# Optimization experiments

Measured on AMD Instinct MI355X. Metric: run time of the kernel, lower is better.

## Reference

```python
import jax, jax.numpy as jnp
import numpy as np

B, S, H = 32, 2048, 1024

def setup_inputs() -> dict:
    key = jax.random.key(0)
    ks = jax.random.split(key, 8)
    s = 1.0 / np.sqrt(H)
    return {
        "query": jax.random.normal(ks[0], (B, 1, H), jnp.float32),
        "keys": jax.random.normal(ks[1], (B, S, H), jnp.float32),
        "Wa_w": jax.random.normal(ks[2], (H, H), jnp.float32) * s,
        "Wa_b": jax.random.normal(ks[3], (H,), jnp.float32) * s,
        "Ua_w": jax.random.normal(ks[4], (H, H), jnp.float32) * s,
        "Ua_b": jax.random.normal(ks[5], (H,), jnp.float32) * s,
        "Va_w": jax.random.normal(ks[6], (1, H), jnp.float32) * s,
        "Va_b": jax.random.normal(ks[7], (1,), jnp.float32) * s,
    }

def reference(query, keys, Wa_w, Wa_b, Ua_w, Ua_b, Va_w, Va_b):
    # Wa(query): (B,1,H); Ua(keys): (B,S,H); broadcast add -> (B,S,H)
    q = jnp.einsum('bqh,oh->bqo', query, Wa_w) + Wa_b
    k = jnp.einsum('bsh,oh->bso', keys, Ua_w) + Ua_b
    h = jnp.tanh(q + k)                              # (B,S,H)
    scores = jnp.einsum('bsh,oh->bso', h, Va_w) + Va_b  # (B,S,1)
    scores = scores[:, :, 0][:, None, :]             # (B,1,S)
    weights = jax.nn.softmax(scores, axis=-1)        # (B,1,S)
    context = jnp.einsum('bqs,bsh->bqh', weights, keys)  # (B,1,H)
    return context, weights
```

## Files before the change

kernel.cpp:

```cpp
#include <hip/hip_runtime.h>
#include <hip/hip_bf16.h>

#define HDIM 1024
#define SEQ  2048
#define BATCH 32
#define M_TOTAL (BATCH * SEQ)
#define BM 256
#define BN 128
#define BK 32
#define NSLICE 16

typedef __bf16 bf16x8 __attribute__((ext_vector_type(8)));
typedef float  f32x4  __attribute__((ext_vector_type(4)));
typedef unsigned short u16;
#define AS1 __attribute__((address_space(1)))
#define AS3 __attribute__((address_space(3)))

__device__ __forceinline__ u16 f2bf(float f) {
    unsigned int u = __float_as_uint(f);
    u += 0x7FFFu + ((u >> 16) & 1u);
    return (u16)(u >> 16);
}

__global__ __launch_bounds__(256) void cvt_kernel(const float* __restrict__ in,
                                                  u16* __restrict__ out) {
    size_t i = ((size_t)blockIdx.x * 256 + threadIdx.x) * 8;
    float4 f0 = *(const float4*)(in + i);
    float4 f1 = *(const float4*)(in + i + 4);
    uint4 v;
    v.x = (unsigned)f2bf(f0.x) | ((unsigned)f2bf(f0.y) << 16);
    v.y = (unsigned)f2bf(f0.z) | ((unsigned)f2bf(f0.w) << 16);
    v.z = (unsigned)f2bf(f1.x) | ((unsigned)f2bf(f1.y) << 16);
    v.w = (unsigned)f2bf(f1.z) | ((unsigned)f2bf(f1.w) << 16);
    *(uint4*)(out + i) = v;
}

__global__ __launch_bounds__(256) void qb_kernel(const float* __restrict__ query,
                                                 const float* __restrict__ Wa_w,
                                                 const float* __restrict__ Wa_b,
                                                 const float* __restrict__ Ua_b,
                                                 float* __restrict__ qb) {
    __shared__ float qs[HDIM];
    const int b = blockIdx.x;
    const int tid = threadIdx.x;
    ((float4*)qs)[tid] = ((const float4*)(query + b * HDIM))[tid];
    __syncthreads();
    const int lane = tid & 63;
    const int w = tid >> 6;
    const int obase = blockIdx.y * 64 + w * 16;
    for (int i = 0; i < 16; i++) {
        int o = obase + i;
        const float4* wrow = (const float4*)(Wa_w + (size_t)o * HDIM);
        float s = 0.f;
        #pragma unroll
        for (int j = 0; j < 4; j++) {
            float4 wv = wrow[j * 64 + lane];
            float4 qv = ((const float4*)qs)[j * 64 + lane];
            s += wv.x * qv.x + wv.y * qv.y + wv.z * qv.z + wv.w * qv.w;
        }
        #pragma unroll
        for (int m = 1; m < 64; m <<= 1) s += __shfl_xor(s, m);
        if (lane == 0) qb[b * HDIM + o] = s + Wa_b[o] + Ua_b[o];
    }
}

__global__ __launch_bounds__(256, 2) void gemm_score_kernel(const u16* __restrict__ keysb,
                                                            const u16* __restrict__ uab,
                                                            const float* __restrict__ qb,
                                                            const float* __restrict__ vaw,
                                                            float* __restrict__ sp) {
    __shared__ __align__(16) u16 As[BM * BK];
    __shared__ __align__(16) u16 Bs[BN * BK];
    const int tid  = threadIdx.x;
    const int lane = tid & 63;
    const int w    = tid >> 6;
    const int m0 = blockIdx.x * BM;
    const int n0 = blockIdx.y * BN;
    const int wave_m = (w & 1) * 128;
    const int wave_n = (w >> 1) * 64;

    f32x4 acc[8][4] = {};

    const int srow = lane >> 2;
    const int scol = (lane & 3) * 8;
    const u16* gA = keysb + (size_t)(m0 + w * 64 + srow) * HDIM + scol;
    const u16* gB = uab   + (size_t)(n0 + w * 32 + srow) * HDIM + scol;
    u16* lA = As + (w * 64) * BK;
    u16* lB = Bs + (w * 32) * BK;

    const int fr = lane & 15;
    const int fq = lane >> 4;

    for (int k0 = 0; k0 < HDIM; k0 += BK) {
        __syncthreads();
        #pragma unroll
        for (int i = 0; i < 4; i++)
            __builtin_amdgcn_global_load_lds((AS1 void*)(gA + k0 + i * 16 * HDIM),
                                             (AS3 void*)(lA + i * 16 * BK), 16, 0, 0);
        #pragma unroll
        for (int i = 0; i < 2; i++)
            __builtin_amdgcn_global_load_lds((AS1 void*)(gB + k0 + i * 16 * HDIM),
                                             (AS3 void*)(lB + i * 16 * BK), 16, 0, 0);
        __syncthreads();

        bf16x8 a[8], b[4];
        #pragma unroll
        for (int i = 0; i < 8; i++)
            a[i] = *(const bf16x8*)(As + (wave_m + i * 16 + fr) * BK + fq * 8);
        #pragma unroll
        for (int i = 0; i < 4; i++)
            b[i] = *(const bf16x8*)(Bs + (wave_n + i * 16 + fr) * BK + fq * 8);
        #pragma unroll
        for (int mi = 0; mi < 8; mi++)
            #pragma unroll
            for (int ni = 0; ni < 4; ni++)
                acc[mi][ni] = __builtin_amdgcn_mfma_f32_16x16x32_bf16(a[mi], b[ni], acc[mi][ni], 0, 0, 0);
    }

    const int bidx = m0 >> 11;
    float qv[4], vv[4];
    #pragma unroll
    for (int ni = 0; ni < 4; ni++) {
        int n_g = n0 + wave_n + ni * 16 + fr;
        qv[ni] = qb[bidx * HDIM + n_g];
        vv[ni] = vaw[n_g];
    }
    const int slice = blockIdx.y * 2 + (w >> 1);
    float* sl = sp + ((size_t)slice * BATCH + bidx) * SEQ;
    #pragma unroll
    for (int mi = 0; mi < 8; mi++) {
        #pragma unroll
        for (int r = 0; r < 4; r++) {
            float p = 0.f;
            #pragma unroll
            for (int ni = 0; ni < 4; ni++) {
                float x = acc[mi][ni][r] + qv[ni];
                float e = __expf(2.f * x);
                p += (1.f - 2.f / (e + 1.f)) * vv[ni];
            }
            p += __shfl_xor(p, 1);
            p += __shfl_xor(p, 2);
            p += __shfl_xor(p, 4);
            p += __shfl_xor(p, 8);
            if (fr == 0) {
                int s_g = (m0 + wave_m + mi * 16 + fq * 4 + r) & (SEQ - 1);
                sl[s_g] = p;
            }
        }
    }
}

__global__ __launch_bounds__(256) void softmax_kernel(const float* __restrict__ sp,
                                                      float* __restrict__ weights,
                                                      float* __restrict__ ctx) {
    __shared__ float red[4];
    const int b = blockIdx.x;
    const int tid = threadIdx.x;
    float4 z = {0.f, 0.f, 0.f, 0.f};
    ((float4*)(ctx + b * HDIM))[tid] = z;
    float v[8];
    float mx = -1e30f;
    #pragma unroll
    for (int i = 0; i < 8; i++) {
        int s = tid + i * 256;
        float a = 0.f;
        #pragma unroll
        for (int j = 0; j < NSLICE; j++) a += sp[((size_t)j * BATCH + b) * SEQ + s];
        v[i] = a;
        mx = fmaxf(mx, a);
    }
    #pragma unroll
    for (int m = 1; m < 64; m <<= 1) mx = fmaxf(mx, __shfl_xor(mx, m));
    if ((tid & 63) == 0) red[tid >> 6] = mx;
    __syncthreads();
    mx = fmaxf(fmaxf(red[0], red[1]), fmaxf(red[2], red[3]));
    float sum = 0.f;
    #pragma unroll
    for (int i = 0; i < 8; i++) { v[i] = __expf(v[i] - mx); sum += v[i]; }
    #pragma unroll
    for (int m = 1; m < 64; m <<= 1) sum += __shfl_xor(sum, m);
    __syncthreads();
    if ((tid & 63) == 0) red[tid >> 6] = sum;
    __syncthreads();
    sum = red[0] + red[1] + red[2] + red[3];
    float inv = 1.f / sum;
    #pragma unroll
    for (int i = 0; i < 8; i++) weights[b * SEQ + tid + i * 256] = v[i] * inv;
}

__global__ __launch_bounds__(256) void context_kernel(const float* __restrict__ keys,
                                                      const float* __restrict__ weights,
                                                      float* __restrict__ ctx) {
    __shared__ float wsm[64];
    const int b = blockIdx.x;
    const int s0 = blockIdx.y * 64;
    const int tid = threadIdx.x;
    if (tid < 64) wsm[tid] = weights[b * SEQ + s0 + tid];
    __syncthreads();
    float ax = 0.f, ay = 0.f, az = 0.f, aw = 0.f;
    const float4* kp = (const float4*)(keys + (size_t)b * SEQ * HDIM + (size_t)s0 * HDIM) + tid;
    #pragma unroll 8
    for (int s = 0; s < 64; s++) {
        float4 kv = kp[s * 256];
        float wv = wsm[s];
        ax += wv * kv.x; ay += wv * kv.y; az += wv * kv.z; aw += wv * kv.w;
    }
    float* o = ctx + b * HDIM + tid * 4;
    atomicAdd(o + 0, ax);
    atomicAdd(o + 1, ay);
    atomicAdd(o + 2, az);
    atomicAdd(o + 3, aw);
}

extern "C" void kernel_launch(void* const* d_in, const int* in_sizes, int n_in,
                              void* d_out, int out_size, void* d_ws, size_t ws_size,
                              hipStream_t stream) {
    const float* query = (const float*)d_in[0];
    const float* keys  = (const float*)d_in[1];
    const float* Wa_w  = (const float*)d_in[2];
    const float* Wa_b  = (const float*)d_in[3];
    const float* Ua_w  = (const float*)d_in[4];
    const float* Ua_b  = (const float*)d_in[5];
    const float* Va_w  = (const float*)d_in[6];
    float* out = (float*)d_out;

    char* ws = (char*)d_ws;
    u16*  keysb = (u16*)ws;
    u16*  uab   = (u16*)(ws + 134217728);
    float* qb   = (float*)(ws + 134217728 + 2097152);
    float* sp   = (float*)(ws + 134217728 + 2097152 + 131072);

    cvt_kernel<<<(BATCH * SEQ * HDIM) / 2048, 256, 0, stream>>>(keys, keysb);
    cvt_kernel<<<(HDIM * HDIM) / 2048, 256, 0, stream>>>(Ua_w, uab);
    qb_kernel<<<dim3(BATCH, HDIM / 64), 256, 0, stream>>>(query, Wa_w, Wa_b, Ua_b, qb);
    gemm_score_kernel<<<dim3(M_TOTAL / BM, HDIM / BN), 256, 0, stream>>>(keysb, uab, qb, Va_w, sp);
    softmax_kernel<<<BATCH, 256, 0, stream>>>(sp, out + BATCH * HDIM, out);
    context_kernel<<<dim3(BATCH, SEQ / 64), 256, 0, stream>>>(keys, out + BATCH * HDIM, out);
}
```

Baseline: 671.9 us.

## Fuse fp32-to-bf16 key conversion into GEMM loads, shrink tile, swizzle LDS

Drops the separate pass that converted the full keys tensor to bf16. The GEMM now loads fp32 keys straight into LDS and converts them to bf16 in registers before the MFMA, which removes the 256MB read plus 128MB write of the conversion pass. To fit the doubled fp32 A tile, BM drops from 256 to 128 and the occupancy hint rises to 3. The grid is reordered so N-blocks sharing an M tile run together, and XOR swizzles are added to LDS accesses to cut bank conflicts. In exchange, the GEMM reads fp32 keys once per N block (8 times in total), which doubles its A-side global traffic, and it adds conversion work inside the inner loop.

```diff
diff --git a/kernel.cpp b/kernel.cpp
--- a/kernel.cpp
+++ b/kernel.cpp
@@ -5,7 +5,7 @@
 #define SEQ  2048
 #define BATCH 32
 #define M_TOTAL (BATCH * SEQ)
-#define BM 256
+#define BM 128
 #define BN 128
 #define BK 32
 #define NSLICE 16
@@ -20,6 +20,15 @@
     unsigned int u = __float_as_uint(f);
     u += 0x7FFFu + ((u >> 16) & 1u);
     return (u16)(u >> 16);
+}
+
+__device__ __forceinline__ bf16x8 cvt8(float4 f0, float4 f1) {
+    union { bf16x8 v; __hip_bfloat162 h[4]; } u;
+    u.h[0] = __float22bfloat162_rn({f0.x, f0.y});
+    u.h[1] = __float22bfloat162_rn({f0.z, f0.w});
+    u.h[2] = __float22bfloat162_rn({f1.x, f1.y});
+    u.h[3] = __float22bfloat162_rn({f1.z, f1.w});
+    return u.v;
 }
 
 __global__ __launch_bounds__(256) void cvt_kernel(const float* __restrict__ in,
@@ -64,54 +73,61 @@
     }
 }
 
-__global__ __launch_bounds__(256, 2) void gemm_score_kernel(const u16* __restrict__ keysb,
+__global__ __launch_bounds__(256, 3) void gemm_score_kernel(const float* __restrict__ keys,
                                                             const u16* __restrict__ uab,
                                                             const float* __restrict__ qb,
                                                             const float* __restrict__ vaw,
                                                             float* __restrict__ sp) {
-    __shared__ __align__(16) u16 As[BM * BK];
-    __shared__ __align__(16) u16 Bs[BN * BK];
+    __shared__ __align__(16) float As[BM * BK];
+    __shared__ __align__(16) u16   Bs[BN * BK];
     const int tid  = threadIdx.x;
     const int lane = tid & 63;
     const int w    = tid >> 6;
-    const int m0 = blockIdx.x * BM;
-    const int n0 = blockIdx.y * BN;
-    const int wave_m = (w & 1) * 128;
+    const int n0 = blockIdx.x * BN;
+    const int m0 = blockIdx.y * BM;
+    const int wave_m = (w & 1) * 64;
     const int wave_n = (w >> 1) * 64;
 
-    f32x4 acc[8][4] = {};
-
-    const int srow = lane >> 2;
-    const int scol = (lane & 3) * 8;
-    const u16* gA = keysb + (size_t)(m0 + w * 64 + srow) * HDIM + scol;
-    const u16* gB = uab   + (size_t)(n0 + w * 32 + srow) * HDIM + scol;
-    u16* lA = As + (w * 64) * BK;
+    f32x4 acc[4][4] = {};
+
+    const int arow = lane >> 3;
+    const int achk = (lane & 7) ^ (arow & 7);
+    const float* gA = keys + (size_t)(m0 + w * 32 + arow) * HDIM + achk * 4;
+    float* lA = As + (w * 32) * BK;
+    const int brow = lane >> 2;
+    const int bchk = (lane & 3) ^ ((lane >> 3) & 3);
+    const u16* gB = uab + (size_t)(n0 + w * 32 + brow) * HDIM + bchk * 8;
     u16* lB = Bs + (w * 32) * BK;
 
     const int fr = lane & 15;
     const int fq = lane >> 4;
+    const int aswz0 = ((2 * fq + 0) ^ (fr & 7)) * 4;
+    const int aswz1 = ((2 * fq + 1) ^ (fr & 7)) * 4;
+    const int bswz  = (fq ^ ((fr >> 1) & 3)) * 8;
 
     for (int k0 = 0; k0 < HDIM; k0 += BK) {
         __syncthreads();
         #pragma unroll
         for (int i = 0; i < 4; i++)
-            __builtin_amdgcn_global_load_lds((AS1 void*)(gA + k0 + i * 16 * HDIM),
-                                             (AS3 void*)(lA + i * 16 * BK), 16, 0, 0);
+            __builtin_amdgcn_global_load_lds((AS1 void*)(gA + k0 + i * 8 * HDIM),
+                                             (AS3 void*)(lA + i * 8 * BK), 16, 0, 0);
         #pragma unroll
         for (int i = 0; i < 2; i++)
             __builtin_amdgcn_global_load_lds((AS1 void*)(gB + k0 + i * 16 * HDIM),
                                              (AS3 void*)(lB + i * 16 * BK), 16, 0, 0);
         __syncthreads();
 
-        bf16x8 a[8], b[4];
-        #pragma unroll
-        for (int i = 0; i < 8; i++)
-            a[i] = *(const bf16x8*)(As + (wave_m + i * 16 + fr) * BK + fq * 8);
-        #pragma unroll
-        for (int i = 0; i < 4; i++)
-            b[i] = *(const bf16x8*)(Bs + (wave_n + i * 16 + fr) * BK + fq * 8);
-        #pragma unroll
-        for (int mi = 0; mi < 8; mi++)
+        bf16x8 a[4], b[4];
+        #pragma unroll
+        for (int i = 0; i < 4; i++) {
+            const float* ar = As + (wave_m + i * 16 + fr) * BK;
+            float4 f0 = *(const float4*)(ar + aswz0);
+            float4 f1 = *(const float4*)(ar + aswz1);
+            a[i] = cvt8(f0, f1);
+            b[i] = *(const bf16x8*)(Bs + (wave_n + i * 16 + fr) * BK + bswz);
+        }
+        #pragma unroll
+        for (int mi = 0; mi < 4; mi++)
             #pragma unroll
             for (int ni = 0; ni < 4; ni++)
                 acc[mi][ni] = __builtin_amdgcn_mfma_f32_16x16x32_bf16(a[mi], b[ni], acc[mi][ni], 0, 0, 0);
@@ -125,10 +141,10 @@
         qv[ni] = qb[bidx * HDIM + n_g];
         vv[ni] = vaw[n_g];
     }
-    const int slice = blockIdx.y * 2 + (w >> 1);
+    const int slice = blockIdx.x * 2 + (w >> 1);
     float* sl = sp + ((size_t)slice * BATCH + bidx) * SEQ;
     #pragma unroll
-    for (int mi = 0; mi < 8; mi++) {
+    for (int mi = 0; mi < 4; mi++) {
         #pragma unroll
         for (int r = 0; r < 4; r++) {
             float p = 0.f;
@@ -225,15 +241,13 @@
     float* out = (float*)d_out;
 
     char* ws = (char*)d_ws;
-    u16*  keysb = (u16*)ws;
-    u16*  uab   = (u16*)(ws + 134217728);
-    float* qb   = (float*)(ws + 134217728 + 2097152);
-    float* sp   = (float*)(ws + 134217728 + 2097152 + 131072);
-
-    cvt_kernel<<<(BATCH * SEQ * HDIM) / 2048, 256, 0, stream>>>(keys, keysb);
+    u16*  uab = (u16*)ws;
+    float* qb = (float*)(ws + 2097152);
+    float* sp = (float*)(ws + 2097152 + 131072);
+
     cvt_kernel<<<(HDIM * HDIM) / 2048, 256, 0, stream>>>(Ua_w, uab);
     qb_kernel<<<dim3(BATCH, HDIM / 64), 256, 0, stream>>>(query, Wa_w, Wa_b, Ua_b, qb);
-    gemm_score_kernel<<<dim3(M_TOTAL / BM, HDIM / BN), 256, 0, stream>>>(keysb, uab, qb, Va_w, sp);
+    gemm_score_kernel<<<dim3(HDIM / BN, M_TOTAL / BM), 256, 0, stream>>>(keys, uab, qb, Va_w, sp);
     softmax_kernel<<<BATCH, 256, 0, stream>>>(sp, out + BATCH * HDIM, out);
     context_kernel<<<dim3(BATCH, SEQ / 64), 256, 0, stream>>>(keys, out + BATCH * HDIM, out);
 }
```

Measured after the change: 644.0 us. 1.04x faster.

## Swap GEMM tile shape and grid order; read bf16 keys in context kernel

Applied to the files above, without the earlier changes.

The GEMM tile changes from 256x128 to 128x256, and the grid is reordered so N-blocks vary fastest. Consecutive blocks then share the same keys rows in cache, and fewer score slices are written. The context kernel now reads the bf16 copy of keys instead of the fp32 original, halving the bytes of its main memory stream. The cost is reduced precision in the context output and more atomic adds per block.

```diff
diff --git a/kernel.cpp b/kernel.cpp
--- a/kernel.cpp
+++ b/kernel.cpp
@@ -5,10 +5,10 @@
 #define SEQ  2048
 #define BATCH 32
 #define M_TOTAL (BATCH * SEQ)
-#define BM 256
-#define BN 128
+#define BM 128
+#define BN 256
 #define BK 32
-#define NSLICE 16
+#define NSLICE 8
 
 typedef __bf16 bf16x8 __attribute__((ext_vector_type(8)));
 typedef float  f32x4  __attribute__((ext_vector_type(4)));
@@ -74,19 +74,19 @@
     const int tid  = threadIdx.x;
     const int lane = tid & 63;
     const int w    = tid >> 6;
-    const int m0 = blockIdx.x * BM;
-    const int n0 = blockIdx.y * BN;
-    const int wave_m = (w & 1) * 128;
-    const int wave_n = (w >> 1) * 64;
-
-    f32x4 acc[8][4] = {};
+    const int n0 = blockIdx.x * BN;
+    const int m0 = blockIdx.y * BM;
+    const int wave_m = (w & 1) * 64;
+    const int wave_n = (w >> 1) * 128;
+
+    f32x4 acc[4][8] = {};
 
     const int srow = lane >> 2;
     const int scol = (lane & 3) * 8;
-    const u16* gA = keysb + (size_t)(m0 + w * 64 + srow) * HDIM + scol;
-    const u16* gB = uab   + (size_t)(n0 + w * 32 + srow) * HDIM + scol;
-    u16* lA = As + (w * 64) * BK;
-    u16* lB = Bs + (w * 32) * BK;
+    const u16* gA = keysb + (size_t)(m0 + w * 32 + srow) * HDIM + scol;
+    const u16* gB = uab   + (size_t)(n0 + w * 64 + srow) * HDIM + scol;
+    u16* lA = As + (w * 32) * BK;
+    u16* lB = Bs + (w * 64) * BK;
 
     const int fr = lane & 15;
     const int fq = lane >> 4;
@@ -94,46 +94,46 @@
     for (int k0 = 0; k0 < HDIM; k0 += BK) {
         __syncthreads();
         #pragma unroll
-        for (int i = 0; i < 4; i++)
+        for (int i = 0; i < 2; i++)
             __builtin_amdgcn_global_load_lds((AS1 void*)(gA + k0 + i * 16 * HDIM),
                                              (AS3 void*)(lA + i * 16 * BK), 16, 0, 0);
         #pragma unroll
-        for (int i = 0; i < 2; i++)
+        for (int i = 0; i < 4; i++)
             __builtin_amdgcn_global_load_lds((AS1 void*)(gB + k0 + i * 16 * HDIM),
                                              (AS3 void*)(lB + i * 16 * BK), 16, 0, 0);
         __syncthreads();
 
-        bf16x8 a[8], b[4];
+        bf16x8 a[4], b[8];
+        #pragma unroll
+        for (int i = 0; i < 4; i++)
+            a[i] = *(const bf16x8*)(As + (wave_m + i * 16 + fr) * BK + fq * 8);
         #pragma unroll
         for (int i = 0; i < 8; i++)
-            a[i] = *(const bf16x8*)(As + (wave_m + i * 16 + fr) * BK + fq * 8);
-        #pragma unroll
-        for (int i = 0; i < 4; i++)
             b[i] = *(const bf16x8*)(Bs + (wave_n + i * 16 + fr) * BK + fq * 8);
         #pragma unroll
-        for (int mi = 0; mi < 8; mi++)
+        for (int mi = 0; mi < 4; mi++)
             #pragma unroll
-            for (int ni = 0; ni < 4; ni++)
+            for (int ni = 0; ni < 8; ni++)
                 acc[mi][ni] = __builtin_amdgcn_mfma_f32_16x16x32_bf16(a[mi], b[ni], acc[mi][ni], 0, 0, 0);
     }
 
     const int bidx = m0 >> 11;
-    float qv[4], vv[4];
-    #pragma unroll
-    for (int ni = 0; ni < 4; ni++) {
+    float qv[8], vv[8];
+    #pragma unroll
+    for (int ni = 0; ni < 8; ni++) {
         int n_g = n0 + wave_n + ni * 16 + fr;
         qv[ni] = qb[bidx * HDIM + n_g];
         vv[ni] = vaw[n_g];
     }
-    const int slice = blockIdx.y * 2 + (w >> 1);
+    const int slice = blockIdx.x * 2 + (w >> 1);
     float* sl = sp + ((size_t)slice * BATCH + bidx) * SEQ;
     #pragma unroll
-    for (int mi = 0; mi < 8; mi++) {
+    for (int mi = 0; mi < 4; mi++) {
         #pragma unroll
         for (int r = 0; r < 4; r++) {
             float p = 0.f;
             #pragma unroll
-            for (int ni = 0; ni < 4; ni++) {
+            for (int ni = 0; ni < 8; ni++) {
                 float x = acc[mi][ni][r] + qv[ni];
                 float e = __expf(2.f * x);
                 p += (1.f - 2.f / (e + 1.f)) * vv[ni];
@@ -188,7 +188,7 @@
     for (int i = 0; i < 8; i++) weights[b * SEQ + tid + i * 256] = v[i] * inv;
 }
 
-__global__ __launch_bounds__(256) void context_kernel(const float* __restrict__ keys,
+__global__ __launch_bounds__(256) void context_kernel(const u16* __restrict__ keysb,
                                                       const float* __restrict__ weights,
                                                       float* __restrict__ ctx) {
     __shared__ float wsm[64];
@@ -197,19 +197,34 @@
     const int tid = threadIdx.x;
     if (tid < 64) wsm[tid] = weights[b * SEQ + s0 + tid];
     __syncthreads();
-    float ax = 0.f, ay = 0.f, az = 0.f, aw = 0.f;
-    const float4* kp = (const float4*)(keys + (size_t)b * SEQ * HDIM + (size_t)s0 * HDIM) + tid;
+    const int hq = tid & 127;
+    const int sh = (tid >> 7) * 32;
+    float a0 = 0.f, a1 = 0.f, a2 = 0.f, a3 = 0.f;
+    float a4 = 0.f, a5 = 0.f, a6 = 0.f, a7 = 0.f;
+    const uint4* kp = (const uint4*)(keysb + (size_t)b * SEQ * HDIM
+                                     + (size_t)(s0 + sh) * HDIM) + hq;
     #pragma unroll 8
-    for (int s = 0; s < 64; s++) {
-        float4 kv = kp[s * 256];
-        float wv = wsm[s];
-        ax += wv * kv.x; ay += wv * kv.y; az += wv * kv.z; aw += wv * kv.w;
-    }
-    float* o = ctx + b * HDIM + tid * 4;
-    atomicAdd(o + 0, ax);
-    atomicAdd(o + 1, ay);
-    atomicAdd(o + 2, az);
-    atomicAdd(o + 3, aw);
+    for (int s = 0; s < 32; s++) {
+        uint4 kv = kp[s * 128];
+        float wv = wsm[sh + s];
+        a0 += wv * __uint_as_float(kv.x << 16);
+        a1 += wv * __uint_as_float(kv.x & 0xFFFF0000u);
+        a2 += wv * __uint_as_float(kv.y << 16);
+        a3 += wv * __uint_as_float(kv.y & 0xFFFF0000u);
+        a4 += wv * __uint_as_float(kv.z << 16);
+        a5 += wv * __uint_as_float(kv.z & 0xFFFF0000u);
+        a6 += wv * __uint_as_float(kv.w << 16);
+        a7 += wv * __uint_as_float(kv.w & 0xFFFF0000u);
+    }
+    float* o = ctx + b * HDIM + hq * 8;
+    atomicAdd(o + 0, a0);
+    atomicAdd(o + 1, a1);
+    atomicAdd(o + 2, a2);
+    atomicAdd(o + 3, a3);
+    atomicAdd(o + 4, a4);
+    atomicAdd(o + 5, a5);
+    atomicAdd(o + 6, a6);
+    atomicAdd(o + 7, a7);
 }
 
 extern "C" void kernel_launch(void* const* d_in, const int* in_sizes, int n_in,
@@ -233,7 +248,7 @@
     cvt_kernel<<<(BATCH * SEQ * HDIM) / 2048, 256, 0, stream>>>(keys, keysb);
     cvt_kernel<<<(HDIM * HDIM) / 2048, 256, 0, stream>>>(Ua_w, uab);
     qb_kernel<<<dim3(BATCH, HDIM / 64), 256, 0, stream>>>(query, Wa_w, Wa_b, Ua_b, qb);
-    gemm_score_kernel<<<dim3(M_TOTAL / BM, HDIM / BN), 256, 0, stream>>>(keysb, uab, qb, Va_w, sp);
+    gemm_score_kernel<<<dim3(HDIM / BN, M_TOTAL / BM), 256, 0, stream>>>(keysb, uab, qb, Va_w, sp);
     softmax_kernel<<<BATCH, 256, 0, stream>>>(sp, out + BATCH * HDIM, out);
-    context_kernel<<<dim3(BATCH, SEQ / 64), 256, 0, stream>>>(keys, out + BATCH * HDIM, out);
-}
+    context_kernel<<<dim3(BATCH, SEQ / 64), 256, 0, stream>>>(keysb, out + BATCH * HDIM, out);
+}
```

Result: no change. 667.1 us (-0.7%).
